# Optimization experiments

Measured on AMD Instinct MI355X. Metric: run time of the kernel, lower is better.

The kernel has to match this reference:

```python
import jax, jax.numpy as jnp
import numpy as np

CODEBOOK_SIZE = 8192
EMBED_DIM = 256


def setup_inputs() -> dict:
    key = jax.random.key(0)
    k_rep, k_cb = jax.random.split(key)
    rep = jax.random.normal(k_rep, (32, 2048, EMBED_DIM), dtype=jnp.float32)
    codebook = jax.random.normal(k_cb, (CODEBOOK_SIZE, EMBED_DIM), dtype=jnp.float32)
    return {"rep": rep, "codebook": codebook}


def reference(rep, codebook):
    # rep: [B, M, D], codebook: [K, D]
    B, M, D = rep.shape
    rep_flat = rep.reshape(-1, D)                                # [B*M, D]
    a2 = jnp.sum(rep_flat * rep_flat, axis=1, keepdims=True)     # [B*M, 1]
    b2 = jnp.sum(codebook * codebook, axis=1)[None, :]           # [1, K]
    ab = rep_flat @ codebook.T                                   # [B*M, K]
    dist = a2 + b2 - 2.0 * ab                                    # [B*M, K]
    idx = jnp.argmin(dist, axis=1).reshape(B, M)                 # [B, M] int
    return idx
```

## Files before the change

### kernel.cpp

```cpp
#include <hip/hip_runtime.h>
#include <stdint.h>

#define KCODES 8192
#define DIM 256
#define BN 128
#define NKT (KCODES / BN)
#define NSTEP (NKT * 4)

typedef _Float16 h16;
typedef __attribute__((ext_vector_type(8))) _Float16 f16x8;
typedef __attribute__((ext_vector_type(4))) float f32x4;

__device__ __forceinline__ void split8(const float* __restrict__ x, f16x8& h, f16x8& l) {
    #pragma unroll
    for (int i = 0; i < 8; ++i) {
        float v = x[i];
        _Float16 hv = (_Float16)v;
        h[i] = hv;
        l[i] = (_Float16)(v - (float)hv);
    }
}

__device__ __forceinline__ unsigned int ford(float f) {
    unsigned int b = __float_as_uint(f);
    return (b & 0x80000000u) ? ~b : (b | 0x80000000u);
}

#define WS_C2H   0u
#define WS_LC    32768u
#define WS_CN    65536u
#define WS_CNT   98304u
#define WS_LIST  98560u
#define WS_KEYS  917504u
#define WS_BPH   2097152u

__global__ __launch_bounds__(256) void prep_kernel(const float* __restrict__ cb,
                                                   h16* __restrict__ Bp,
                                                   float* __restrict__ c2h,
                                                   float* __restrict__ lc,
                                                   float* __restrict__ cn) {
    const int tid = blockIdx.x * 256 + threadIdx.x;
    const int code = tid >> 5;
    const int grp = tid & 31;
    float x[8];
    *(float4*)&x[0] = *(const float4*)(cb + (size_t)code * DIM + grp * 8);
    *(float4*)&x[4] = *(const float4*)(cb + (size_t)code * DIM + grp * 8 + 4);
    f16x8 hh;
    float s = 0.f, sr = 0.f;
    #pragma unroll
    for (int i = 0; i < 8; ++i) {
        float v = x[i];
        _Float16 hv = (_Float16)v;
        hh[i] = hv;
        s += v * v;
        float rho = v - (float)hv;
        sr += rho * rho;
    }
    const int kt = code >> 7, c = code & 127;
    const int h = c >> 6, cl = c & 63;
    const int n = cl >> 4, c15 = cl & 15;
    const int cp = grp >> 3, j = (grp >> 2) & 1, g = grp & 3;
    const int lane = g * 16 + c15;
    const size_t off = (((size_t)((kt * 4 + cp) * 2 + h) * 8) + (n * 2 + j)) * 512 + lane * 8;
    *(f16x8*)(Bp + off) = hh;

    #pragma unroll
    for (int o = 16; o > 0; o >>= 1) { s += __shfl_xor(s, o); sr += __shfl_xor(sr, o); }
    if (grp == 0) {
        c2h[code] = 0.5f * s;
        cn[code] = sqrtf(s);
        lc[code] = sqrtf(sr);
    }
}

__global__ __launch_bounds__(256) void vq_pass1(
    const float* __restrict__ rep, const float* __restrict__ cb,
    const h16* __restrict__ Bp, const float* __restrict__ c2h,
    const float* __restrict__ lcA, const float* __restrict__ cnA,
    int* __restrict__ out, int* __restrict__ cnt, int* __restrict__ list) {

    __shared__ __align__(16) h16 lds[4][2][8][512];

    const int t = threadIdx.x;
    const int lane = t & 63;
    const int c15 = lane & 15;
    const int g = lane >> 4;
    const int w = t >> 6;
    const int rh = w >> 1;
    const int h = w & 1;
    const int brow = blockIdx.x * 64;

    f16x8 ah[2][8];
    float hnr[2][4], rnr[2][4];
    #pragma unroll
    for (int m = 0; m < 2; ++m) {
        const float* ar = rep + (size_t)(brow + rh * 32 + m * 16 + c15) * DIM + g * 8;
        float hs = 0.f, rs = 0.f;
        #pragma unroll
        for (int ch = 0; ch < 8; ++ch) {
            float x[8];
            *(float4*)&x[0] = *(const float4*)(ar + ch * 32);
            *(float4*)&x[4] = *(const float4*)(ar + ch * 32 + 4);
            #pragma unroll
            for (int i = 0; i < 8; ++i) {
                _Float16 hv = (_Float16)x[i];
                ah[m][ch][i] = hv;
                float hf = (float)hv;
                hs += hf * hf;
                float rho = x[i] - hf;
                rs += rho * rho;
            }
        }
        hs += __shfl_xor(hs, 16); hs += __shfl_xor(hs, 32);
        rs += __shfl_xor(rs, 16); rs += __shfl_xor(rs, 32);
        float hn = sqrtf(hs), rn = sqrtf(rs);
        #pragma unroll
        for (int r = 0; r < 4; ++r) {
            hnr[m][r] = __shfl(hn, g * 4 + r);
            rnr[m][r] = __shfl(rn, g * 4 + r);
        }
    }

    f32x4 acc[2][4];
    float u1v[2][4], u2v[2][4], Dl[4], Dc[4], D2[4];
    int u1i[2][4];
    #pragma unroll
    for (int m = 0; m < 2; ++m)
        #pragma unroll
        for (int n = 0; n < 4; ++n) {
            #pragma unroll
            for (int r = 0; r < 4; ++r) acc[m][n][r] = 0.f;
            u1v[m][n] = -3.4e38f; u2v[m][n] = -3.4e38f; u1i[m][n] = 0;
        }

    auto issueStep = [&](int S, int buf) {
        const h16* src = Bp + ((size_t)(S * 2 + h) * 8) * 512 + lane * 8;
        #pragma unroll
        for (int f = 0; f < 8; ++f)
            __builtin_amdgcn_global_load_lds(
                (const __attribute__((address_space(1))) uint32_t*)(src + f * 512),
                (__attribute__((address_space(3))) uint32_t*)(&lds[w][buf][f][lane * 8]),
                16, 0, 0);
    };

    asm volatile("s_waitcnt vmcnt(0)" ::: "memory");
    issueStep(0, 0);

    #pragma unroll 1
    for (int kt = 0; kt < NKT; ++kt) {
        const int ktbase = kt * BN;
        #pragma unroll
        for (int cp = 0; cp < 4; ++cp) {
            const int S = kt * 4 + cp;
            const int cur = cp & 1;
            if (cp == 0) {
                #pragma unroll
                for (int n = 0; n < 4; ++n) {
                    const int col = ktbase + h * 64 + n * 16 + c15;
                    Dl[n] = lcA[col];
                    Dc[n] = cnA[col];
                    D2[n] = 0.012f - c2h[col];
                }
            }
            if (S + 1 < NSTEP) issueStep(S + 1, cur ^ 1);
            if (S == NSTEP - 1) asm volatile("s_waitcnt vmcnt(0)" ::: "memory");
            else                asm volatile("s_waitcnt vmcnt(8)" ::: "memory");
            __builtin_amdgcn_sched_barrier(0);

            #pragma unroll
            for (int j = 0; j < 2; ++j) {
                const int ch = cp * 2 + j;
                #pragma unroll
                for (int n = 0; n < 4; ++n) {
                    f16x8 bh = *(const f16x8*)&lds[w][cur][n * 2 + j][lane * 8];
                    #pragma unroll
                    for (int m = 0; m < 2; ++m)
                        acc[m][n] = __builtin_amdgcn_mfma_f32_16x16x32_f16(ah[m][ch], bh, acc[m][n], 0, 0, 0);
                }
            }

            if (cp == 3) {
                #pragma unroll
                for (int n = 0; n < 4; ++n) {
                    const int col = ktbase + h * 64 + n * 16 + c15;
                    #pragma unroll
                    for (int m = 0; m < 2; ++m)
                        #pragma unroll
                        for (int r = 0; r < 4; ++r) {
                            float u = fmaf(hnr[m][r], Dl[n],
                                      fmaf(rnr[m][r], Dc[n], acc[m][n][r] + D2[n]));
                            if (u > u1v[m][r]) { u2v[m][r] = u1v[m][r]; u1v[m][r] = u; u1i[m][r] = col; }
                            else if (u > u2v[m][r]) u2v[m][r] = u;
                            acc[m][n][r] = 0.f;
                        }
                }
            }
        }
    }

    __syncthreads();
    float* sv1 = (float*)&lds[0][0][0][0];
    int* si1 = (int*)((char*)&lds[0][0][0][0] + 1024);
    float* sv2 = (float*)((char*)&lds[0][0][0][0] + 2048);
    int* cand_s = (int*)((char*)&lds[0][0][0][0] + 4096);
    float* thr_s = (float*)((char*)&lds[0][0][0][0] + 4608);
    #pragma unroll
    for (int m = 0; m < 2; ++m)
        #pragma unroll
        for (int r = 0; r < 4; ++r) {
            float a1 = u1v[m][r], a2 = u2v[m][r];
            int a1i = u1i[m][r];
            #pragma unroll
            for (int mask = 1; mask <= 8; mask <<= 1) {
                float b1 = __shfl_xor(a1, mask);
                int b1i = __shfl_xor(a1i, mask);
                float b2 = __shfl_xor(a2, mask);
                if (b1 > a1) { a2 = fmaxf(a1, b2); a1 = b1; a1i = b1i; }
                else         { a2 = fmaxf(b1, a2); }
            }
            if (c15 == 0) {
                const int rl = rh * 32 + m * 16 + g * 4 + r;
                sv1[rl * 2 + h] = a1;
                si1[rl * 2 + h] = a1i;
                sv2[rl * 2 + h] = a2;
            }
        }
    __syncthreads();
    if (t < 64) {
        float a1 = sv1[t * 2], a2 = sv2[t * 2];
        int a1i = si1[t * 2];
        float b1 = sv1[t * 2 + 1], b2 = sv2[t * 2 + 1];
        int b1i = si1[t * 2 + 1];
        float u1, u2; int u1idx;
        if (b1 > a1) { u1 = b1; u1idx = b1i; u2 = fmaxf(a1, b2); }
        else         { u1 = a1; u1idx = a1i; u2 = fmaxf(b1, a2); }
        cand_s[t] = u1idx;
        thr_s[t] = u2;
        out[brow + t] = u1idx;
    }
    __syncthreads();

    #pragma unroll 1
    for (int i = 0; i < 16; ++i) {
        const int rl = w * 16 + i;
        const int grow = brow + rl;
        const int ci = cand_s[rl];
        const float4 rv = *(const float4*)(rep + (size_t)grow * DIM + lane * 4);
        const float4 cv = *(const float4*)(cb + (size_t)ci * DIM + lane * 4);
        float p = rv.x * cv.x + rv.y * cv.y + rv.z * cv.z + rv.w * cv.w;
        #pragma unroll
        for (int off = 32; off > 0; off >>= 1) p += __shfl_down(p, off);
        if (lane == 0) {
            float sex = p - c2h[ci];
            if (!(sex > thr_s[rl])) {
                int pos = atomicAdd(cnt, 1);
                list[pos] = grow;
            }
        }
    }
}

__global__ __launch_bounds__(256) void rescan_kernel(
    const float* __restrict__ rep, const float* __restrict__ cb,
    const float* __restrict__ c2h, const int* __restrict__ cnt_p,
    const int* __restrict__ list, unsigned long long* __restrict__ keys) {

    const int cnt = *cnt_p;
    const int base = blockIdx.x * 64;
    if (base >= cnt) return;
    const int nrows = min(64, cnt - base);
    const int ktbase = (int)blockIdx.y * BN;

    __shared__ __align__(16) h16 lds[2][BN * 64];
    const int t = threadIdx.x;
    const int lane = t & 63;
    const int w = t >> 6;
    const int c15 = lane & 15;
    const int g = lane >> 4;
    const int wrow = w * 16;

    const int aslot = wrow + c15;
    const int grow = list[base + (aslot < nrows ? aslot : 0)];
    f16x8 ah[8], al[8];
    {
        const float* ar = rep + (size_t)grow * DIM + g * 8;
        #pragma unroll
        for (int ch = 0; ch < 8; ++ch) {
            float x[8];
            *(float4*)&x[0] = *(const float4*)(ar + ch * 32);
            *(float4*)&x[4] = *(const float4*)(ar + ch * 32 + 4);
            split8(x, ah[ch], al[ch]);
        }
    }
    f32x4 acc[8];
    float cc[8];
    #pragma unroll
    for (int n = 0; n < 8; ++n) {
        #pragma unroll
        for (int r = 0; r < 4; ++r) acc[n][r] = 0.f;
        cc[n] = c2h[ktbase + n * 16 + c15];
    }

    const int scol = t >> 1;
    const int dslot = t & 1;
    float breg[16];
    auto loadB = [&](int ch) {
        const float* src = cb + (size_t)(ktbase + scol) * DIM + ch * 32 + dslot * 16;
        #pragma unroll
        for (int i = 0; i < 4; ++i) *(float4*)&breg[i * 4] = *(const float4*)(src + i * 4);
    };
    auto writeB = [&](int buf) {
        #pragma unroll
        for (int half = 0; half < 2; ++half) {
            f16x8 hh, ll;
            split8(&breg[half * 8], hh, ll);
            const int s = dslot * 2 + half;
            *(f16x8*)&lds[buf][scol * 64 + ((s ^ (scol & 7)) << 3)] = hh;
            *(f16x8*)&lds[buf][scol * 64 + (((s + 4) ^ (scol & 7)) << 3)] = ll;
        }
    };

    loadB(0);
    writeB(0);
    loadB(1);
    __syncthreads();

    #pragma unroll
    for (int chunk = 0; chunk < 8; ++chunk) {
        const int buf = chunk & 1;
        if (chunk != 7) writeB(buf ^ 1);
        if (chunk <= 5) loadB(chunk + 2);
        #pragma unroll
        for (int n = 0; n < 8; ++n) {
            const int bb2 = (n * 16 + c15) * 64;
            f16x8 bh = *(const f16x8*)&lds[buf][bb2 + ((g ^ (lane & 7)) << 3)];
            f16x8 bl = *(const f16x8*)&lds[buf][bb2 + (((4 + g) ^ (lane & 7)) << 3)];
            acc[n] = __builtin_amdgcn_mfma_f32_16x16x32_f16(ah[chunk], bh, acc[n], 0, 0, 0);
            acc[n] = __builtin_amdgcn_mfma_f32_16x16x32_f16(ah[chunk], bl, acc[n], 0, 0, 0);
            acc[n] = __builtin_amdgcn_mfma_f32_16x16x32_f16(al[chunk], bh, acc[n], 0, 0, 0);
            acc[n] = __builtin_amdgcn_mfma_f32_16x16x32_f16(al[chunk], bl, acc[n], 0, 0, 0);
        }
        __syncthreads();
    }

    #pragma unroll
    for (int r = 0; r < 4; ++r) {
        float bv = -3.4e38f;
        int bi = 0;
        #pragma unroll
        for (int n = 0; n < 8; ++n) {
            float s2 = acc[n][r] - cc[n];
            const int col = ktbase + n * 16 + c15;
            if (s2 > bv) { bv = s2; bi = col; }
        }
        #pragma unroll
        for (int mask = 1; mask <= 8; mask <<= 1) {
            float ov = __shfl_xor(bv, mask);
            int oi = __shfl_xor(bi, mask);
            if (ov > bv || (ov == bv && oi < bi)) { bv = ov; bi = oi; }
        }
        const int oslot = wrow + g * 4 + r;
        if (c15 == 0 && oslot < nrows) {
            unsigned long long key =
                ((unsigned long long)ford(bv) << 32) | (unsigned int)(~(unsigned int)bi);
            atomicMax(&keys[list[base + oslot]], key);
        }
    }
}

__global__ __launch_bounds__(256) void writeback_kernel(
    const int* __restrict__ cnt_p, const int* __restrict__ list,
    const unsigned long long* __restrict__ keys, int* __restrict__ out) {
    int i = blockIdx.x * 256 + threadIdx.x;
    if (i >= *cnt_p) return;
    int row = list[i];
    out[row] = (int)(~(unsigned int)(keys[row] & 0xFFFFFFFFull));
}

extern "C" void kernel_launch(void* const* d_in, const int* in_sizes, int n_in,
                              void* d_out, int out_size, void* d_ws, size_t ws_size,
                              hipStream_t stream) {
    const float* rep = (const float*)d_in[0];
    const float* cb = (const float*)d_in[1];
    const int N = in_sizes[0] / DIM;
    const int K = in_sizes[1] / DIM;
    (void)K;
    char* ws = (char*)d_ws;
    float* c2h = (float*)(ws + WS_C2H);
    float* lc  = (float*)(ws + WS_LC);
    float* cn  = (float*)(ws + WS_CN);
    int* cnt   = (int*)(ws + WS_CNT);
    int* list  = (int*)(ws + WS_LIST);
    unsigned long long* keys = (unsigned long long*)(ws + WS_KEYS);
    h16* Bph   = (h16*)(ws + WS_BPH);
    int* out = (int*)d_out;

    hipMemsetAsync(ws + WS_CNT, 0, 64, stream);
    hipMemsetAsync(keys, 0, (size_t)N * sizeof(unsigned long long), stream);
    prep_kernel<<<dim3(KCODES * 32 / 256), dim3(256), 0, stream>>>(cb, Bph, c2h, lc, cn);
    vq_pass1<<<dim3(N / 64), dim3(256), 0, stream>>>(rep, cb, Bph, c2h, lc, cn, out, cnt, list);
    rescan_kernel<<<dim3(N / 64, NKT), dim3(256), 0, stream>>>(rep, cb, c2h, cnt, list, keys);
    writeback_kernel<<<dim3(N / 256), dim3(256), 0, stream>>>(cnt, list, keys, out);
}
```

Before: 523.0 us.

## Load codebook fragments directly into registers instead of staging through LDS

Replaces the global_load_lds double-buffered staging of the packed codebook with direct global-to-register f16x8 loads into a two-slot register buffer. Shared memory shrinks to small arrays used only for the final reduction. This removes the LDS round trip and the explicit vmcnt waits, and lets the compiler schedule waits itself. In exchange it adds register pressure (16 extra f16x8 vectors) and loses the precise manual wait control, which may reduce occupancy or expose load latency.

```diff
diff --git a/kernel.cpp b/kernel.cpp
--- a/kernel.cpp
+++ b/kernel.cpp
@@ -79,7 +79,11 @@
     const float* __restrict__ lcA, const float* __restrict__ cnA,
     int* __restrict__ out, int* __restrict__ cnt, int* __restrict__ list) {
 
-    __shared__ __align__(16) h16 lds[4][2][8][512];
+    __shared__ float sv1[128];
+    __shared__ int si1[128];
+    __shared__ float sv2[128];
+    __shared__ int cand_s[64];
+    __shared__ float thr_s[64];
 
     const int t = threadIdx.x;
     const int lane = t & 63;
@@ -122,6 +126,7 @@
     }
 
     f32x4 acc[2][4];
+    f16x8 breg[2][8];
     float u1v[2][4], u2v[2][4], Dl[4], Dc[4], D2[4];
     int u1i[2][4];
     #pragma unroll
@@ -133,18 +138,12 @@
             u1v[m][n] = -3.4e38f; u2v[m][n] = -3.4e38f; u1i[m][n] = 0;
         }
 
-    auto issueStep = [&](int S, int buf) {
-        const h16* src = Bp + ((size_t)(S * 2 + h) * 8) * 512 + lane * 8;
+    {
+        const h16* src = Bp + (size_t)h * 4096 + lane * 8;
         #pragma unroll
         for (int f = 0; f < 8; ++f)
-            __builtin_amdgcn_global_load_lds(
-                (const __attribute__((address_space(1))) uint32_t*)(src + f * 512),
-                (__attribute__((address_space(3))) uint32_t*)(&lds[w][buf][f][lane * 8]),
-                16, 0, 0);
-    };
-
-    asm volatile("s_waitcnt vmcnt(0)" ::: "memory");
-    issueStep(0, 0);
+            breg[0][f] = *(const f16x8*)(src + f * 512);
+    }
 
     #pragma unroll 1
     for (int kt = 0; kt < NKT; ++kt) {
@@ -152,7 +151,7 @@
         #pragma unroll
         for (int cp = 0; cp < 4; ++cp) {
             const int S = kt * 4 + cp;
-            const int cur = cp & 1;
+            const int p = cp & 1;
             if (cp == 0) {
                 #pragma unroll
                 for (int n = 0; n < 4; ++n) {
@@ -162,21 +161,21 @@
                     D2[n] = 0.012f - c2h[col];
                 }
             }
-            if (S + 1 < NSTEP) issueStep(S + 1, cur ^ 1);
-            if (S == NSTEP - 1) asm volatile("s_waitcnt vmcnt(0)" ::: "memory");
-            else                asm volatile("s_waitcnt vmcnt(8)" ::: "memory");
-            __builtin_amdgcn_sched_barrier(0);
+            if (S + 1 < NSTEP) {
+                const h16* src = Bp + (size_t)((S + 1) * 2 + h) * 4096 + lane * 8;
+                #pragma unroll
+                for (int f = 0; f < 8; ++f)
+                    breg[p ^ 1][f] = *(const f16x8*)(src + f * 512);
+            }
 
             #pragma unroll
             for (int j = 0; j < 2; ++j) {
                 const int ch = cp * 2 + j;
                 #pragma unroll
-                for (int n = 0; n < 4; ++n) {
-                    f16x8 bh = *(const f16x8*)&lds[w][cur][n * 2 + j][lane * 8];
+                for (int n = 0; n < 4; ++n)
                     #pragma unroll
                     for (int m = 0; m < 2; ++m)
-                        acc[m][n] = __builtin_amdgcn_mfma_f32_16x16x32_f16(ah[m][ch], bh, acc[m][n], 0, 0, 0);
-                }
+                        acc[m][n] = __builtin_amdgcn_mfma_f32_16x16x32_f16(ah[m][ch], breg[p][n * 2 + j], acc[m][n], 0, 0, 0);
             }
 
             if (cp == 3) {
@@ -198,12 +197,6 @@
         }
     }
 
-    __syncthreads();
-    float* sv1 = (float*)&lds[0][0][0][0];
-    int* si1 = (int*)((char*)&lds[0][0][0][0] + 1024);
-    float* sv2 = (float*)((char*)&lds[0][0][0][0] + 2048);
-    int* cand_s = (int*)((char*)&lds[0][0][0][0] + 4096);
-    float* thr_s = (float*)((char*)&lds[0][0][0][0] + 4608);
     #pragma unroll
     for (int m = 0; m < 2; ++m)
         #pragma unroll
```

After: 656.3 us. 25.5% more time.
